# Kernel tuning notes

Hardware: AMD Instinct MI355X
Metric: run time of the kernel (lower is better)

The kernel has to match this reference:

```python
import jax, jax.numpy as jnp
import numpy as np

B, C, H, W = 8, 256, 64, 64

def setup_inputs() -> dict:
    key = jax.random.key(0)
    ks = jax.random.split(key, 8)
    s = 0.02  # keep logits in a sane range
    return {
        "x": jax.random.normal(ks[0], (B, C, H, W), jnp.float32),
        "motion_info": jax.random.normal(ks[1], (B, C, H, W), jnp.float32),
        "wq": jax.random.normal(ks[2], (C, C), jnp.float32) * s,
        "bq": jax.random.normal(ks[3], (C,), jnp.float32) * s,
        "wk": jax.random.normal(ks[4], (C, C), jnp.float32) * s,
        "bk": jax.random.normal(ks[5], (C,), jnp.float32) * s,
        "wv": jax.random.normal(ks[6], (C, C), jnp.float32) * s,
        "bv": jax.random.normal(ks[7], (C,), jnp.float32) * s,
    }

def reference(x, motion_info, wq, bq, wk, bk, wv, bv):
    b, c, h, w = x.shape
    n = h * w
    scale = c ** (-0.5)
    # 1x1 convs == channel-mixing GEMMs; flatten spatial to tokens
    xf = x.reshape(b, c, n)              # [B,C,N]
    mf = motion_info.reshape(b, c, n)    # [B,C,N]
    q = jnp.einsum('dc,bcn->bdn', wq, xf) + bq[None, :, None]
    k = jnp.einsum('dc,bcn->bdn', wk, mf) + bk[None, :, None]
    v = jnp.einsum('dc,bcn->bdn', wv, mf) + bv[None, :, None]
    # attn[b,i,j] = <q[:,i], k[:,j]> * scale, softmax over j
    attn = jax.nn.softmax(jnp.einsum('bci,bcj->bij', q, k) * scale, axis=-1)
    # out[b,c,i] = sum_j v[b,c,j] * attn[b,i,j]
    out = jnp.einsum('bcj,bij->bci', v, attn)
    return out.reshape(b, c, h, w)
```

## Files before the change

### kernel.cpp

```cpp
#include <hip/hip_runtime.h>
#include <hip/hip_bf16.h>

#define BATCH 8
#define CH    256
#define NTOK  4096

typedef __bf16 bf16_t;
typedef __bf16 bf16x8 __attribute__((ext_vector_type(8)));
typedef __bf16 bf16x4 __attribute__((ext_vector_type(4)));
typedef float  fx4    __attribute__((ext_vector_type(4)));


__global__ __launch_bounds__(256, 2) void proj_kernel(
    const float* __restrict__ x, const float* __restrict__ motion,
    const float* __restrict__ wq, const float* __restrict__ bq,
    const float* __restrict__ wk, const float* __restrict__ bk,
    const float* __restrict__ wv, const float* __restrict__ bv,
    bf16_t* __restrict__ qg, bf16_t* __restrict__ kg, bf16_t* __restrict__ vg)
{
    const int mat = blockIdx.y;
    const int b   = blockIdx.x & 7;
    const int n0  = (blockIdx.x >> 3) * 64;
    const float* __restrict__ src  = (mat == 0) ? x  : motion;
    const float* __restrict__ W    = (mat == 0) ? wq : (mat == 1 ? wk : wv);
    const float* __restrict__ bias = (mat == 0) ? bq : (mat == 1 ? bk : bv);

    __shared__ __align__(16) unsigned char smem[55296 + 1024];
    bf16_t* Xt    = (bf16_t*)smem;
    bf16_t* Wl    = (bf16_t*)(smem + 33792);
    bf16_t* OutL  = (bf16_t*)smem;
    float*  biasL = (float*)(smem + 55296);

    const int tid  = threadIdx.x;
    const int w    = tid >> 6;
    const int lane = tid & 63;
    const int l16  = lane & 15;
    const int quad = lane >> 4;

    biasL[tid] = bias[tid];

    for (int it = 0; it < 16; ++it) {
        const int c  = it * 16 + (tid >> 4);
        const int j4 = (tid & 15) * 4;
        const float4 v = *(const float4*)&src[((size_t)b * CH + c) * NTOK + n0 + j4];
        Xt[(j4 + 0) * 264 + c] = (bf16_t)v.x;
        Xt[(j4 + 1) * 264 + c] = (bf16_t)v.y;
        Xt[(j4 + 2) * 264 + c] = (bf16_t)v.z;
        Xt[(j4 + 3) * 264 + c] = (bf16_t)v.w;
    }

    fx4 acc[16];
    for (int i = 0; i < 16; ++i) acc[i] = (fx4){0.f, 0.f, 0.f, 0.f};

    for (int cs = 0; cs < 8; ++cs) {
        for (int it = 0; it < 8; ++it) {
            const int d  = it * 32 + (tid >> 3);
            const int c4 = (tid & 7) * 4;
            const float4 v = *(const float4*)&W[(size_t)d * CH + cs * 32 + c4];
            bf16x4 pk;
            pk[0] = (bf16_t)v.x; pk[1] = (bf16_t)v.y;
            pk[2] = (bf16_t)v.z; pk[3] = (bf16_t)v.w;
            *(bf16x4*)&Wl[d * 40 + c4] = pk;
        }
        __syncthreads();
        const bf16x8 af = *(const bf16x8*)&Xt[(w * 16 + l16) * 264 + cs * 32 + quad * 8];
        for (int dp = 0; dp < 16; ++dp) {
            const bf16x8 bf = *(const bf16x8*)&Wl[(dp * 16 + l16) * 40 + quad * 8];
            acc[dp] = __builtin_amdgcn_mfma_f32_16x16x32_bf16(af, bf, acc[dp], 0, 0, 0);
        }
        __syncthreads();
    }

    const float qs = (mat == 0) ? 0.0625f : 1.0f;
    for (int dp = 0; dp < 16; ++dp) {
        const int d = dp * 16 + l16;
        const float bb = biasL[d];
        bf16x4 pk;
        for (int r = 0; r < 4; ++r)
            pk[r] = (bf16_t)((acc[dp][r] + bb) * qs);
        *(bf16x4*)&OutL[d * 72 + w * 16 + quad * 4] = pk;
    }
    __syncthreads();

    if (mat < 2) {
        bf16_t* __restrict__ G = (mat == 0) ? qg : kg;
        for (int it = 0; it < 8; ++it) {
            const int n  = it * 8 + (tid >> 5);
            const int d8 = (tid & 31) * 8;
            bf16x8 vv;
            for (int k = 0; k < 8; ++k) vv[k] = OutL[(d8 + k) * 72 + n];
            *(bf16x8*)&G[((size_t)b * NTOK + n0 + n) * CH + d8] = vv;
        }
    } else {
        for (int it = 0; it < 8; ++it) {
            const int d  = it * 32 + (tid >> 3);
            const int n8 = (tid & 7) * 8;
            const bf16x8 vv = *(const bf16x8*)&OutL[d * 72 + n8];
            *(bf16x8*)&vg[((size_t)b * CH + d) * NTOK + n0 + n8] = vv;
        }
    }
}

__global__ __launch_bounds__(256, 3) void attn_kernel(
    const bf16_t* __restrict__ qg, const bf16_t* __restrict__ kg,
    const bf16_t* __restrict__ vg, float* __restrict__ out)
{
    const int b  = blockIdx.x & 7;
    const int i0 = (blockIdx.x >> 3) * 64;

    __shared__ __align__(16) unsigned char smem[42752];
    bf16_t* Kt   = (bf16_t*)smem;
    bf16_t* Vt   = (bf16_t*)(smem + 16896);
    bf16_t* Pb   = (bf16_t*)(smem + 37376);
    float*  lred = (float*)(smem + 42496);

    const int tid = threadIdx.x;
    const int w = tid >> 6, lane = tid & 63, l16 = lane & 15, quad = lane >> 4;

    bf16x8 qf[8];
    {
        const bf16_t* qb = qg + ((size_t)b * NTOK + i0 + w * 16 + l16) * CH;
        for (int cs = 0; cs < 8; ++cs)
            qf[cs] = *(const bf16x8*)&qb[cs * 32 + quad * 8];
    }

    fx4 oacc[16];
    for (int i = 0; i < 16; ++i) oacc[i] = (fx4){0.f, 0.f, 0.f, 0.f};
    float rs[4] = {0.f, 0.f, 0.f, 0.f};

    bf16_t* PbW = Pb + w * (16 * 40);

    for (int jt = 0; jt < 128; ++jt) {
        const int j0 = jt * 32;
        for (int it = 0; it < 4; ++it) {
            const int j  = it * 8 + (tid >> 5);
            const int c8 = (tid & 31) * 8;
            *(bf16x8*)&Kt[j * 264 + c8] =
                *(const bf16x8*)&kg[((size_t)b * NTOK + j0 + j) * CH + c8];
        }
        for (int it = 0; it < 4; ++it) {
            const int c  = it * 64 + (tid >> 2);
            const int j8 = (tid & 3) * 8;
            *(bf16x8*)&Vt[c * 40 + j8] =
                *(const bf16x8*)&vg[((size_t)b * CH + c) * NTOK + j0 + j8];
        }
        __syncthreads();

        for (int jp = 0; jp < 2; ++jp) {
            fx4 s = (fx4){0.f, 0.f, 0.f, 0.f};
            for (int cs = 0; cs < 8; ++cs) {
                const bf16x8 kf =
                    *(const bf16x8*)&Kt[(jp * 16 + l16) * 264 + cs * 32 + quad * 8];
                s = __builtin_amdgcn_mfma_f32_16x16x32_bf16(qf[cs], kf, s, 0, 0, 0);
            }
            for (int r = 0; r < 4; ++r) {
                const float p = __expf(s[r]);
                rs[r] += p;
                PbW[(quad * 4 + r) * 40 + jp * 16 + l16] = (bf16_t)p;
            }
        }
        __syncthreads();

        const bf16x8 pf = *(const bf16x8*)&PbW[l16 * 40 + quad * 8];
        for (int cp = 0; cp < 16; ++cp) {
            const bf16x8 vf = *(const bf16x8*)&Vt[(cp * 16 + l16) * 40 + quad * 8];
            oacc[cp] = __builtin_amdgcn_mfma_f32_16x16x32_bf16(vf, pf, oacc[cp], 0, 0, 0);
        }
        __syncthreads();
    }

    for (int r = 0; r < 4; ++r) {
        float v = rs[r];
        v += __shfl_xor(v, 1);
        v += __shfl_xor(v, 2);
        v += __shfl_xor(v, 4);
        v += __shfl_xor(v, 8);
        rs[r] = v;
    }
    if (l16 == 0)
        for (int r = 0; r < 4; ++r) lred[w * 16 + quad * 4 + r] = rs[r];
    __syncthreads();
    const float linv = 1.0f / lred[w * 16 + l16];

    const int i = i0 + w * 16 + l16;
    for (int cp = 0; cp < 16; ++cp) {
        for (int r = 0; r < 4; ++r) {
            const int c = cp * 16 + quad * 4 + r;
            out[((size_t)b * CH + c) * NTOK + i] = oacc[cp][r] * linv;
        }
    }
}

extern "C" void kernel_launch(void* const* d_in, const int* in_sizes, int n_in,
                              void* d_out, int out_size, void* d_ws, size_t ws_size,
                              hipStream_t stream) {
    const float* x  = (const float*)d_in[0];
    const float* mi = (const float*)d_in[1];
    const float* wq = (const float*)d_in[2];
    const float* bq = (const float*)d_in[3];
    const float* wk = (const float*)d_in[4];
    const float* bk = (const float*)d_in[5];
    const float* wv = (const float*)d_in[6];
    const float* bv = (const float*)d_in[7];

    bf16_t* qg = (bf16_t*)d_ws;
    bf16_t* kg = qg + (size_t)BATCH * NTOK * CH;
    bf16_t* vg = kg + (size_t)BATCH * NTOK * CH;

    dim3 pgrid(BATCH * (NTOK / 64), 3);
    proj_kernel<<<pgrid, 256, 0, stream>>>(x, mi, wq, bq, wk, bk, wv, bv, qg, kg, vg);
    attn_kernel<<<BATCH * (NTOK / 64), 256, 0, stream>>>(qg, kg, vg, (float*)d_out);
}
```

Measured before the change: 395.6 us.

## Double-buffer K via direct global-to-LDS loads and re-split attention warps 2x2

Rewrites the attention kernel to load K and V tiles with global_load_lds straight into XOR-swizzled, unpadded LDS, double-buffering K so the next tile's load overlaps the current tile's compute. Warps are re-partitioned 2x2: for QK^T each warp covers 32 query rows by 16 keys, and for PV each warp covers 32 query rows by 128 channels, so each loaded K/V fragment feeds two MFMAs. Row sums are combined across warp halves through LDS at the end. LDS use grows, and launch bounds drop occupancy from 3 to 2 blocks per CU.

Result: faster. 332.1 us (-16.1%).

```diff
diff --git a/kernel.cpp b/kernel.cpp
--- a/kernel.cpp
+++ b/kernel.cpp
@@ -9,6 +9,11 @@
 typedef __bf16 bf16x8 __attribute__((ext_vector_type(8)));
 typedef __bf16 bf16x4 __attribute__((ext_vector_type(4)));
 typedef float  fx4    __attribute__((ext_vector_type(4)));
+
+#define GLOAD_LDS16(gptr, lptr) \
+    __builtin_amdgcn_global_load_lds( \
+        (const __attribute__((address_space(1))) void*)(gptr), \
+        (__attribute__((address_space(3))) void*)(lptr), 16, 0, 0)
 
 
 __global__ __launch_bounds__(256, 2) void proj_kernel(
@@ -101,92 +106,158 @@
     }
 }
 
-__global__ __launch_bounds__(256, 3) void attn_kernel(
+__global__ __launch_bounds__(256, 2) void attn_kernel(
     const bf16_t* __restrict__ qg, const bf16_t* __restrict__ kg,
     const bf16_t* __restrict__ vg, float* __restrict__ out)
 {
     const int b  = blockIdx.x & 7;
     const int i0 = (blockIdx.x >> 3) * 64;
 
-    __shared__ __align__(16) unsigned char smem[42752];
-    bf16_t* Kt   = (bf16_t*)smem;
-    bf16_t* Vt   = (bf16_t*)(smem + 16896);
-    bf16_t* Pb   = (bf16_t*)(smem + 37376);
-    float*  lred = (float*)(smem + 42496);
-
-    const int tid = threadIdx.x;
-    const int w = tid >> 6, lane = tid & 63, l16 = lane & 15, quad = lane >> 4;
-
-    bf16x8 qf[8];
-    {
-        const bf16_t* qb = qg + ((size_t)b * NTOK + i0 + w * 16 + l16) * CH;
+    __shared__ __align__(16) unsigned char smem[54784];
+    bf16_t* const K0   = (bf16_t*)smem;
+    bf16_t* const K1   = (bf16_t*)(smem + 16384);
+    bf16_t* const Vb   = (bf16_t*)(smem + 32768);
+    bf16_t* const P    = (bf16_t*)(smem + 49152);
+    float*  const lred = (float*)(smem + 54272);
+
+    const int tid  = threadIdx.x;
+    const int w    = tid >> 6;
+    const int lane = tid & 63;
+    const int l16  = lane & 15;
+    const int quad = lane >> 4;
+    const int ih   = w & 1;
+    const int jh   = w >> 1;
+    const int ch   = w & 1;
+    const int is2  = w >> 1;
+    const int w4   = w * 4;
+
+    bf16x8 qf[2][8];
+    #pragma unroll
+    for (int isub = 0; isub < 2; ++isub) {
+        const bf16_t* qb = qg + ((size_t)b * NTOK + i0 + ih * 32 + isub * 16 + l16) * CH;
+        #pragma unroll
         for (int cs = 0; cs < 8; ++cs)
-            qf[cs] = *(const bf16x8*)&qb[cs * 32 + quad * 8];
-    }
-
-    fx4 oacc[16];
-    for (int i = 0; i < 16; ++i) oacc[i] = (fx4){0.f, 0.f, 0.f, 0.f};
-    float rs[4] = {0.f, 0.f, 0.f, 0.f};
-
-    bf16_t* PbW = Pb + w * (16 * 40);
-
-    for (int jt = 0; jt < 128; ++jt) {
-        const int j0 = jt * 32;
+            qf[isub][cs] = *(const bf16x8*)(qb + cs * 32 + quad * 8);
+    }
+
+    fx4 oacc[8][2];
+    #pragma unroll
+    for (int i = 0; i < 8; ++i) {
+        oacc[i][0] = (fx4){0.f, 0.f, 0.f, 0.f};
+        oacc[i][1] = (fx4){0.f, 0.f, 0.f, 0.f};
+    }
+    float rs0[4] = {0.f, 0.f, 0.f, 0.f};
+    float rs1[4] = {0.f, 0.f, 0.f, 0.f};
+
+    const int jrow = jh * 16 + l16;
+    const int sxk  = l16 & 7;
+    const int svo  = (quad ^ (l16 & 3)) * 8;
+
+    #pragma unroll
+    for (int it = 0; it < 4; ++it) {
+        const int N   = w4 + it;
+        const int kj  = 2 * N + (lane >> 5);
+        const int ksl = (lane & 31) ^ (kj & 7);
+        GLOAD_LDS16(kg + (((size_t)b * NTOK + kj) << 8) + ksl * 8, K0 + N * 512);
+    }
+    __syncthreads();
+
+    auto tile = [&](bf16_t* const Kc, bf16_t* const Kn, const int t) {
+        const int j0 = t * 32;
+        #pragma unroll
         for (int it = 0; it < 4; ++it) {
-            const int j  = it * 8 + (tid >> 5);
-            const int c8 = (tid & 31) * 8;
-            *(bf16x8*)&Kt[j * 264 + c8] =
-                *(const bf16x8*)&kg[((size_t)b * NTOK + j0 + j) * CH + c8];
-        }
-        for (int it = 0; it < 4; ++it) {
-            const int c  = it * 64 + (tid >> 2);
-            const int j8 = (tid & 3) * 8;
-            *(bf16x8*)&Vt[c * 40 + j8] =
-                *(const bf16x8*)&vg[((size_t)b * CH + c) * NTOK + j0 + j8];
-        }
-        __syncthreads();
-
-        for (int jp = 0; jp < 2; ++jp) {
-            fx4 s = (fx4){0.f, 0.f, 0.f, 0.f};
+            const int N   = w4 + it;
+            const int vc  = N * 16 + (lane >> 2);
+            const int vsl = (lane & 3) ^ (vc & 3);
+            GLOAD_LDS16(vg + (((size_t)b * CH + vc) << 12) + j0 + vsl * 8,
+                        Vb + N * 512);
+        }
+        if (t + 1 < 128) {
+            #pragma unroll
+            for (int it = 0; it < 4; ++it) {
+                const int N   = w4 + it;
+                const int kj  = 2 * N + (lane >> 5);
+                const int ksl = (lane & 31) ^ (kj & 7);
+                GLOAD_LDS16(kg + (((size_t)b * NTOK + j0 + 32 + kj) << 8) + ksl * 8,
+                            Kn + N * 512);
+            }
+        }
+
+        fx4 s0 = (fx4){0.f, 0.f, 0.f, 0.f};
+        fx4 s1 = (fx4){0.f, 0.f, 0.f, 0.f};
+        {
+            const bf16_t* krow = Kc + jrow * 256;
+            #pragma unroll
             for (int cs = 0; cs < 8; ++cs) {
-                const bf16x8 kf =
-                    *(const bf16x8*)&Kt[(jp * 16 + l16) * 264 + cs * 32 + quad * 8];
-                s = __builtin_amdgcn_mfma_f32_16x16x32_bf16(qf[cs], kf, s, 0, 0, 0);
-            }
+                const bf16x8 kf = *(const bf16x8*)(krow + (((cs * 4 + quad) ^ sxk) * 8));
+                s0 = __builtin_amdgcn_mfma_f32_16x16x32_bf16(qf[0][cs], kf, s0, 0, 0, 0);
+                s1 = __builtin_amdgcn_mfma_f32_16x16x32_bf16(qf[1][cs], kf, s1, 0, 0, 0);
+            }
+        }
+        {
+            bf16_t* prow = P + (ih * 32 + quad * 4) * 40 + jrow;
+            #pragma unroll
             for (int r = 0; r < 4; ++r) {
-                const float p = __expf(s[r]);
-                rs[r] += p;
-                PbW[(quad * 4 + r) * 40 + jp * 16 + l16] = (bf16_t)p;
-            }
-        }
-        __syncthreads();
-
-        const bf16x8 pf = *(const bf16x8*)&PbW[l16 * 40 + quad * 8];
-        for (int cp = 0; cp < 16; ++cp) {
-            const bf16x8 vf = *(const bf16x8*)&Vt[(cp * 16 + l16) * 40 + quad * 8];
-            oacc[cp] = __builtin_amdgcn_mfma_f32_16x16x32_bf16(vf, pf, oacc[cp], 0, 0, 0);
-        }
-        __syncthreads();
-    }
-
+                const float p0 = __expf(s0[r]);
+                const float p1 = __expf(s1[r]);
+                rs0[r] += p0;
+                rs1[r] += p1;
+                prow[r * 40]       = (bf16_t)p0;
+                prow[r * 40 + 640] = (bf16_t)p1;
+            }
+        }
+        __syncthreads();
+
+        {
+            const bf16x8 pf0 = *(const bf16x8*)(P + (is2 * 32 + l16) * 40 + quad * 8);
+            const bf16x8 pf1 = *(const bf16x8*)(P + (is2 * 32 + 16 + l16) * 40 + quad * 8);
+            const bf16_t* vbase = Vb + (ch * 128 + l16) * 32 + svo;
+            #pragma unroll
+            for (int cp8 = 0; cp8 < 8; ++cp8) {
+                const bf16x8 vf = *(const bf16x8*)(vbase + cp8 * 512);
+                oacc[cp8][0] = __builtin_amdgcn_mfma_f32_16x16x32_bf16(vf, pf0, oacc[cp8][0], 0, 0, 0);
+                oacc[cp8][1] = __builtin_amdgcn_mfma_f32_16x16x32_bf16(vf, pf1, oacc[cp8][1], 0, 0, 0);
+            }
+        }
+        __syncthreads();
+    };
+
+    #pragma unroll 1
+    for (int t = 0; t < 128; t += 2) {
+        tile(K0, K1, t);
+        tile(K1, K0, t + 1);
+    }
+
+    #pragma unroll
     for (int r = 0; r < 4; ++r) {
-        float v = rs[r];
-        v += __shfl_xor(v, 1);
-        v += __shfl_xor(v, 2);
-        v += __shfl_xor(v, 4);
-        v += __shfl_xor(v, 8);
-        rs[r] = v;
-    }
-    if (l16 == 0)
-        for (int r = 0; r < 4; ++r) lred[w * 16 + quad * 4 + r] = rs[r];
+        float v0 = rs0[r], v1 = rs1[r];
+        v0 += __shfl_xor(v0, 1); v0 += __shfl_xor(v0, 2);
+        v0 += __shfl_xor(v0, 4); v0 += __shfl_xor(v0, 8);
+        v1 += __shfl_xor(v1, 1); v1 += __shfl_xor(v1, 2);
+        v1 += __shfl_xor(v1, 4); v1 += __shfl_xor(v1, 8);
+        rs0[r] = v0; rs1[r] = v1;
+    }
+    if (l16 == 0) {
+        #pragma unroll
+        for (int r = 0; r < 4; ++r) {
+            lred[jh * 64 + ih * 32 + quad * 4 + r]      = rs0[r];
+            lred[jh * 64 + ih * 32 + 16 + quad * 4 + r] = rs1[r];
+        }
+    }
     __syncthreads();
-    const float linv = 1.0f / lred[w * 16 + l16];
-
-    const int i = i0 + w * 16 + l16;
-    for (int cp = 0; cp < 16; ++cp) {
+
+    const int   row0  = is2 * 32 + l16;
+    const float linv0 = 1.0f / (lred[row0] + lred[64 + row0]);
+    const float linv1 = 1.0f / (lred[row0 + 16] + lred[64 + row0 + 16]);
+
+    const size_t obase = (size_t)b * CH * NTOK + i0 + is2 * 32 + l16;
+    #pragma unroll
+    for (int cp8 = 0; cp8 < 8; ++cp8) {
+        const int c0 = (ch * 8 + cp8) * 16 + quad * 4;
+        #pragma unroll
         for (int r = 0; r < 4; ++r) {
-            const int c = cp * 16 + quad * 4 + r;
-            out[((size_t)b * CH + c) * NTOK + i] = oacc[cp][r] * linv;
+            out[obase + (size_t)(c0 + r) * NTOK]      = oacc[cp8][0][r] * linv0;
+            out[obase + (size_t)(c0 + r) * NTOK + 16] = oacc[cp8][1][r] * linv1;
         }
     }
 }
```
